# Optimization experiments

Measured on AMD Instinct MI355X. Metric: run time of the kernel, lower is better.

## Reference

```python
import jax, jax.numpy as jnp
import numpy as np

N, Q, C, T = 32, 300, 92, 32  # batch, queries, classes, targets-per-image
L_CLS, L_IOU, L_L1 = 1.0, 2.0, 5.0


def _cxcywh_to_xyxy(b):
    cx, cy, w, h = b[..., 0], b[..., 1], b[..., 2], b[..., 3]
    return jnp.stack([cx - 0.5 * w, cy - 0.5 * h, cx + 0.5 * w, cy + 0.5 * h], axis=-1)


def _generalized_box_iou(a, b):
    # a: [P,4] xyxy, b: [M,4] xyxy -> [P,M]
    area_a = (a[:, 2] - a[:, 0]) * (a[:, 3] - a[:, 1])
    area_b = (b[:, 2] - b[:, 0]) * (b[:, 3] - b[:, 1])
    lt = jnp.maximum(a[:, None, :2], b[None, :, :2])
    rb = jnp.minimum(a[:, None, 2:], b[None, :, 2:])
    wh = jnp.clip(rb - lt, 0.0)
    inter = wh[..., 0] * wh[..., 1]
    union = area_a[:, None] + area_b[None, :] - inter
    iou = inter / union
    lt_c = jnp.minimum(a[:, None, :2], b[None, :, :2])
    rb_c = jnp.maximum(a[:, None, 2:], b[None, :, 2:])
    wh_c = jnp.clip(rb_c - lt_c, 0.0)
    area_c = wh_c[..., 0] * wh_c[..., 1]
    return iou - (area_c - union) / area_c


def _cost_matrix(pred_logits, pred_boxes, tgt_labels, tgt_boxes):
    out_prob = jax.nn.softmax(pred_logits.reshape(-1, C), axis=-1)  # [N*Q, C]
    out_bbox = pred_boxes.reshape(-1, 4)                            # [N*Q, 4]
    cost_class = -out_prob[:, tgt_labels]                           # [N*Q, N*T]
    cost_bbox = jnp.sum(jnp.abs(out_bbox[:, None, :] - tgt_boxes[None, :, :]), axis=-1)
    cost_giou = -_generalized_box_iou(_cxcywh_to_xyxy(out_bbox), _cxcywh_to_xyxy(tgt_boxes))
    cost = L_L1 * cost_bbox + L_CLS * cost_class + L_IOU * cost_giou
    return cost.reshape(N, Q, N * T)


def _lsa(cost):
    # Jonker-Volgenant shortest augmenting path (e-maxx), cost: [n, m], n <= m.
    # Returns col4row: for each row, the assigned column.
    n, m = cost.shape
    INF = np.inf
    u = np.zeros(n + 1)
    v = np.zeros(m + 1)
    p = np.zeros(m + 1, dtype=np.int64)   # p[j] = row assigned to column j (1-based)
    way = np.zeros(m + 1, dtype=np.int64)
    for i in range(1, n + 1):
        p[0] = i
        j0 = 0
        minv = np.full(m + 1, INF)
        used = np.zeros(m + 1, dtype=bool)
        while True:
            used[j0] = True
            i0 = p[j0]
            free = ~used[1:]
            cur = cost[i0 - 1] - u[i0] - v[1:]
            upd = free & (cur < minv[1:])
            minv[1:][upd] = cur[upd]
            way[1:][upd] = j0
            j1 = 1 + int(np.argmin(np.where(free, minv[1:], INF)))
            delta = minv[j1]
            used_idx = np.nonzero(used)[0]
            u[p[used_idx]] += delta
            v[used_idx] -= delta
            minv[1:][free] -= delta
            j0 = j1
            if p[j0] == 0:
                break
        while j0:
            j1 = way[j0]
            p[j0] = p[j1]
            j0 = j1
    ans = np.full(n, -1, dtype=np.int64)
    js = np.nonzero(p[1:])[0]
    ans[p[1:][js] - 1] = js
    return ans


def _multiplier(cost):
    c_np = np.asarray(jax.device_get(cost))  # [N, Q, N*T]
    mult = np.zeros_like(c_np)
    for i in range(N):
        block = c_np[i, :, i * T:(i + 1) * T]  # [Q, T], sample i's own targets
        q_of_t = _lsa(block.T)                 # for each target, matched query
        # NOTE: faithfully replicates the original code's `count = 0` reset,
        # so columns are indexed locally (first T columns of the global axis).
        mult[i, q_of_t, np.arange(T)] = 1.0
    return jnp.asarray(mult)


def setup_inputs() -> dict:
    key = jax.random.key(0)
    k1, k2, k3, k4 = jax.random.split(key, 4)
    return {
        "pred_logits": jax.random.normal(k1, (N, Q, C), dtype=jnp.float32),
        "pred_boxes": jax.random.uniform(k2, (N, Q, 4), dtype=jnp.float32),
        "tgt_labels": jax.random.randint(k3, (N * T,), 0, C, dtype=jnp.int64),
        "tgt_boxes": jax.random.uniform(k4, (N * T, 4), dtype=jnp.float32),
    }


def reference(pred_logits, pred_boxes, tgt_labels, tgt_boxes):
    cost = _cost_matrix(pred_logits, pred_boxes, tgt_labels, tgt_boxes)
    mult = _multiplier(cost)
    return jnp.sum(cost * mult)
```

## Files before the change

kernel.cpp:

```cpp
#include <hip/hip_runtime.h>
#include <cfloat>
#include <cmath>

#define Nn 32
#define Qq 300
#define Cc 92
#define Tt 32
#define KCOLS 5
#define GSZ 10
#define GCOLS 30
#define AUCTION_ROUNDS 10
#define AUCTION_EPS 1e-3f

#define SLICES 8
#define RPS 38
#define CTHREADS 256
#define ATHREADS 320
#define FTHREADS 256

#define DIAG_OFF   0
#define MXIS_OFF   (Nn * Tt * Qq)
#define STATE_OFF  (MXIS_OFF + 2 * Nn * Qq)
#define STATE_STRIDE 640

__device__ inline float wave_min_bcast(float x) {
#define DPPMIN(ctrl) { int _t = __builtin_amdgcn_update_dpp( \
        __float_as_int(x), __float_as_int(x), ctrl, 0xf, 0xf, false); \
        x = fminf(x, __int_as_float(_t)); }
    DPPMIN(0x111) DPPMIN(0x112) DPPMIN(0x114) DPPMIN(0x118)
    DPPMIN(0x142) DPPMIN(0x143)
#undef DPPMIN
    return __int_as_float(__builtin_amdgcn_readlane(__float_as_int(x), 63));
}

__device__ inline int sel5i(const int a[KCOLS], int k) {
    int r = a[0];
    if (k == 1) r = a[1];
    if (k == 2) r = a[2];
    if (k == 3) r = a[3];
    if (k == 4) r = a[4];
    return r;
}

__device__ inline float readlane_f(float v, int lane) {
    return __int_as_float(__builtin_amdgcn_readlane(__float_as_int(v), lane));
}

__device__ inline float det_cost_real(float cx, float cy, float w, float h,
                                      float bcx, float bcy, float bw, float bh,
                                      float cls) {
    const float ax0 = cx - 0.5f * w, ay0 = cy - 0.5f * h;
    const float ax1 = cx + 0.5f * w, ay1 = cy + 0.5f * h;
    const float areaA = (ax1 - ax0) * (ay1 - ay0);

    const float l1 = fabsf(cx - bcx) + fabsf(cy - bcy) +
                     fabsf(w - bw) + fabsf(h - bh);

    const float bx0 = bcx - 0.5f * bw, by0 = bcy - 0.5f * bh;
    const float bx1 = bcx + 0.5f * bw, by1 = bcy + 0.5f * bh;
    const float areaB = (bx1 - bx0) * (by1 - by0);

    const float ltx = fmaxf(ax0, bx0), lty = fmaxf(ay0, by0);
    const float rbx = fminf(ax1, bx1), rby = fminf(ay1, by1);
    const float iw = fmaxf(rbx - ltx, 0.f), ih = fmaxf(rby - lty, 0.f);
    const float inter = iw * ih;
    const float uni = areaA + areaB - inter;
    const float iou = inter / uni;

    const float ex0 = fminf(ax0, bx0), ey0 = fminf(ay0, by0);
    const float ex1 = fmaxf(ax1, bx1), ey1 = fmaxf(ay1, by1);
    const float areaC = fmaxf(ex1 - ex0, 0.f) * fmaxf(ey1 - ey0, 0.f);
    const float giou = iou - (areaC - uni) / areaC;

    return 5.f * l1 + cls - 2.f * giou;
}

__global__ __launch_bounds__(CTHREADS) void cost_kernel(
    const float* __restrict__ logits,
    const float* __restrict__ pboxes,
    const int*   __restrict__ tlabels,
    const float* __restrict__ tboxes,
    float* __restrict__ ws)
{
    const int bs = blockIdx.x;
    const int b = bs >> 3, s = bs & 7;
    const int q0 = s * RPS;
    const int nq = min(RPS, Qq - q0);

    __shared__ float2 s_mxis[RPS];
    __shared__ float  s_tb[Tt * 4];
    __shared__ int    s_tl[Tt];

    const int tid = threadIdx.x;
    if (tid < Tt * 4) s_tb[tid] = tboxes[b * Tt * 4 + tid];
    if (tid < Tt)     s_tl[tid] = tlabels[b * Tt + tid];

    const int r = tid >> 2, j = tid & 3;
    if (r < nq) {
        const float* row = logits + ((size_t)(b * Qq) + q0 + r) * Cc;
        float mj = -FLT_MAX;
#pragma unroll
        for (int c = 0; c < Cc; c += 4) mj = fmaxf(mj, row[c + j]);
        const float ma = fmaxf(mj, __shfl_xor(mj, 1, 4));
        const float mx = fmaxf(ma, __shfl_xor(ma, 2, 4));
        float sj = 0.f;
#pragma unroll
        for (int c = 0; c < Cc; c += 4) sj += __expf(row[c + j] - mx);
        const float sa   = sj + __shfl_xor(sj, 1, 4);
        const float ssum = sa + __shfl_xor(sa, 2, 4);
        if (j == 0) {
            const float2 mi = make_float2(mx, 1.f / ssum);
            s_mxis[r] = mi;
            reinterpret_cast<float2*>(ws + MXIS_OFF)[b * Qq + q0 + r] = mi;
        }
    }
    __syncthreads();

    float* diagb = ws + DIAG_OFF + (size_t)b * (Tt * Qq);
    for (int e = tid; e < Tt * RPS; e += CTHREADS) {
        const int t = e / RPS, lq = e - t * RPS;
        const int q = q0 + lq;
        if (q < Qq) {
            const float2 mi = s_mxis[lq];
            const float cls =
                -__expf(logits[((size_t)(b * Qq) + q) * Cc + s_tl[t]] - mi.x) * mi.y;
            const float4 pbv = reinterpret_cast<const float4*>(pboxes)[b * Qq + q];
            diagb[t * Qq + q] = det_cost_real(pbv.x, pbv.y, pbv.z, pbv.w,
                                              s_tb[t * 4 + 0], s_tb[t * 4 + 1],
                                              s_tb[t * 4 + 2], s_tb[t * 4 + 3], cls);
        }
    }
}

__global__ __launch_bounds__(ATHREADS) void auction_kernel(
    float* __restrict__ ws)
{
    const int b = blockIdx.x;
    const int tid = threadIdx.x;

    __shared__ float s_diag[Tt * Qq];
    __shared__ float s_v[Qq];
    __shared__ float s_u[Tt + 1];
    __shared__ int   s_colrow[Qq];
    __shared__ unsigned long long s_bid64[Qq];
    __shared__ float s_pm1[ATHREADS], s_pm2[ATHREADS];
    __shared__ int   s_pa[ATHREADS];
    __shared__ unsigned s_mask;

    {
        const float4* src = reinterpret_cast<const float4*>(
            ws + DIAG_OFF + (size_t)b * (Tt * Qq));
        float4* dst = reinterpret_cast<float4*>(s_diag);
#pragma unroll 2
        for (int g = tid; g < (Tt * Qq) / 4; g += ATHREADS) dst[g] = src[g];
    }
    if (tid < Qq)  { s_v[tid] = 0.f; s_colrow[tid] = 0; }
    if (tid == 0)  s_mask = 0xffffffffu;
    __syncthreads();

    const int grp = tid / GSZ;
    const int g   = tid - grp * GSZ;
    for (int round = 0; round < AUCTION_ROUNDS; ++round) {
        const unsigned msk = s_mask;
        if (msk == 0) break;
        for (int jj = tid; jj < Qq; jj += ATHREADS) s_bid64[jj] = 0ull;

        if (grp < Tt && (msk & (1u << grp))) {
            const float* rowp = &s_diag[grp * Qq];
            float m1 = INFINITY, m2 = INFINITY; int a1 = 0;
            const int c0 = g * GCOLS;
#pragma unroll
            for (int jj = 0; jj < GCOLS; ++jj) {
                const int cidx = c0 + jj;
                const float c = rowp[cidx] - s_v[cidx];
                if (c < m1) { m2 = m1; m1 = c; a1 = cidx + 1; }
                else if (c < m2) m2 = c;
            }
            s_pm1[tid] = m1; s_pm2[tid] = m2; s_pa[tid] = a1;
        }
        __syncthreads();

        float g1 = 0.f, g2 = 0.f; int j1 = 0;
        unsigned long long mypk = 0ull;
        if (tid < Tt && (msk & (1u << tid))) {
            float best = INFINITY, second = INFINITY, bm2 = INFINITY;
            int ba = 0;
            const int base = tid * GSZ;
#pragma unroll
            for (int q = 0; q < GSZ; ++q) {
                const float v = s_pm1[base + q];
                if (v < best) {
                    second = best; best = v;
                    ba = s_pa[base + q]; bm2 = s_pm2[base + q];
                } else if (v < second) second = v;
            }
            g1 = best; g2 = fminf(second, bm2); j1 = ba;
            mypk = ((unsigned long long)(__float_as_uint(g2 - g1) + 1u) << 32)
                   | (unsigned)(0xffffffffu - (unsigned)(tid + 1));
            atomicMax(&s_bid64[j1 - 1], mypk);
        }
        __syncthreads();

        if (tid < Tt && (msk & (1u << tid))) {
            const int row = tid + 1;
            const float eps = (round < 2) ? 0.f : AUCTION_EPS;
            if (s_bid64[j1 - 1] == mypk) {
                const int old = s_colrow[j1 - 1];
                s_colrow[j1 - 1] = row;
                s_v[j1 - 1] -= (g2 - g1) + eps;
                s_u[row] = g2;
                atomicAnd(&s_mask, ~(1u << tid));
                if (old) atomicOr(&s_mask, 1u << (old - 1));
            } else {
                s_u[row] = g1;
            }
        }
        __syncthreads();
    }

    __syncthreads();
    float* st  = ws + STATE_OFF + (size_t)b * STATE_STRIDE;
    int*   sti = reinterpret_cast<int*>(st + 334);
    for (int jj = tid; jj < Qq; jj += ATHREADS) {
        st[jj]  = s_v[jj];
        sti[jj] = s_colrow[jj];
    }
    if (tid >= 1 && tid <= Tt) st[300 + tid] = s_u[tid];
    if (tid == 0) *reinterpret_cast<unsigned*>(st + 634) = s_mask;
}

__global__ __launch_bounds__(FTHREADS) void finish_kernel(
    const float* __restrict__ logits,
    const float* __restrict__ pboxes,
    const int*   __restrict__ tlabels,
    const float* __restrict__ tboxes,
    const float* __restrict__ ws,
    float* __restrict__ out)
{
    const int b = blockIdx.x;
    const int tid = threadIdx.x;

    __shared__ float s_diag[Tt * Qq];
    __shared__ int   pairs[Tt];

    {
        const float4* src = reinterpret_cast<const float4*>(
            ws + DIAG_OFF + (size_t)b * (Tt * Qq));
        float4* dst = reinterpret_cast<float4*>(s_diag);
#pragma unroll 2
        for (int g = tid; g < (Tt * Qq) / 4; g += FTHREADS) dst[g] = src[g];
    }
    __syncthreads();

    if (tid >= 64) return;
    const int lane = tid;
    const bool inval4 = (lane + 256) >= Qq;

    const float* st  = ws + STATE_OFF + (size_t)b * STATE_STRIDE;
    const int*   sti = reinterpret_cast<const int*>(st + 334);

    float u_reg = (lane >= 1 && lane <= Tt) ? st[300 + lane] : 0.f;
    float v_r[KCOLS]; int p_r[KCOLS];
#pragma unroll
    for (int k = 0; k < KCOLS; ++k) {
        const int jj = lane + 64 * k;
        v_r[k] = (jj < Qq) ? st[jj]  : 0.f;
        p_r[k] = (jj < Qq) ? sti[jj] : 0;
    }
    const unsigned mask0 = *reinterpret_cast<const unsigned*>(st + 634);

    for (unsigned rem = mask0; rem; rem &= rem - 1) {
        const int i = __ffs(rem);

        float minv_r[KCOLS], vmask[KCOLS], am[KCOLS];
        int way_r[KCOLS];
#pragma unroll
        for (int k = 0; k < KCOLS; ++k) {
            minv_r[k] = FLT_MAX; way_r[k] = 0;
            const bool inv = (k == 4) && inval4;
            vmask[k] = inv ? -INFINITY : v_r[k];
            am[k]    = inv ?  INFINITY : 0.f;
        }
        float markg = 0.f;
        int   ent = 0;
        int   j0 = 0, i0 = i;
        float du = 0.f - readlane_f(u_reg, i);
        int   jfinal = 0;
        float Dfinal = 0.f;

        const float* rowp = &s_diag[(i0 - 1) * Qq + lane];
        float c0 = rowp[0], c1 = rowp[64], c2 = rowp[128], c3 = rowp[192],
              c4 = rowp[256];

        while (true) {
            const float cc[KCOLS] = {c0, c1, c2, c3, c4};
            float sv[KCOLS];
#pragma unroll
            for (int k = 0; k < KCOLS; ++k) {
                const float cur = (cc[k] + du) - vmask[k];
                const bool lt = cur < minv_r[k];
                way_r[k]  = lt ? j0  : way_r[k];
                minv_r[k] = lt ? cur : minv_r[k];
                sv[k] = minv_r[k] + am[k];
            }
            float val = sv[0];
            int   kb  = 0;
#pragma unroll
            for (int k = 1; k < KCOLS; ++k)
                if (sv[k] < val) { val = sv[k]; kb = k; }

            const float gmin = wave_min_bcast(val);
            const unsigned long long mask = __ballot(val == gmin);
            const int src = __ffsll((long long)mask) - 1;
            const int colid = lane + 1 + (kb << 6);
            const int pk = (sel5i(p_r, kb) << 16) | colid;
            const int got = __builtin_amdgcn_readlane(pk, src);
            const int j1   = got & 0xffff;
            const int rowm = got >> 16;

            const int k1 = (j1 - 1) >> 6;
            const bool own = (lane == ((j1 - 1) & 63));
#pragma unroll
            for (int k = 0; k < KCOLS; ++k)
                if (own && k == k1) { vmask[k] = -INFINITY; am[k] = INFINITY; }

            if (rowm == 0) { jfinal = j1; Dfinal = gmin; break; }

            i0 = rowm; j0 = j1;
            rowp = &s_diag[(i0 - 1) * Qq + lane];
            c0 = rowp[0]; c1 = rowp[64]; c2 = rowp[128]; c3 = rowp[192];
            c4 = rowp[256];
            du = gmin - readlane_f(u_reg, i0);
            markg = (lane == rowm) ? gmin : markg;
            ent   = (lane == rowm) ? 1    : ent;
        }

#pragma unroll
        for (int k = 0; k < KCOLS; ++k) {
            bool usedk = (am[k] == INFINITY);
            if (k == 4) usedk = usedk && !inval4;
            v_r[k] -= usedk ? (Dfinal - minv_r[k]) : 0.f;
        }
        u_reg += (lane == i) ? Dfinal : (ent ? (Dfinal - markg) : 0.f);

        int jj = jfinal;
        while (jj) {
            const int ow = (jj - 1) & 63, kk = (jj - 1) >> 6;
            const int jprev = __builtin_amdgcn_readlane(sel5i(way_r, kk), ow);
            int pnew;
            if (jprev == 0) pnew = i;
            else pnew = __builtin_amdgcn_readlane(sel5i(p_r, (jprev - 1) >> 6),
                                                  (jprev - 1) & 63);
            const bool own = (lane == ow);
#pragma unroll
            for (int k = 0; k < KCOLS; ++k) if (own && k == kk) p_r[k] = pnew;
            jj = jprev;
        }
    }

#pragma unroll
    for (int k = 0; k < KCOLS; ++k)
        if (p_r[k]) pairs[p_r[k] - 1] = lane + 64 * k;
    __threadfence_block();

    float part = 0.f;
    if (lane < Tt) {
        const int q = pairs[lane];
        const float2 mi =
            reinterpret_cast<const float2*>(ws + MXIS_OFF)[b * Qq + q];
        const float cls =
            -__expf(logits[((size_t)(b * Qq) + q) * Cc + tlabels[lane]] - mi.x) * mi.y;
        const float4 pbv = reinterpret_cast<const float4*>(pboxes)[b * Qq + q];
        const float4 tbv = reinterpret_cast<const float4*>(tboxes)[lane];
        part = det_cost_real(pbv.x, pbv.y, pbv.z, pbv.w,
                             tbv.x, tbv.y, tbv.z, tbv.w, cls);
    }
    for (int off = 32; off > 0; off >>= 1) part += __shfl_down(part, off);
    if (lane == 0) atomicAdd(out, part);
}

extern "C" void kernel_launch(void* const* d_in, const int* in_sizes, int n_in,
                              void* d_out, int out_size, void* d_ws, size_t ws_size,
                              hipStream_t stream) {
    const float* logits  = (const float*)d_in[0];
    const float* pboxes  = (const float*)d_in[1];
    const int*   tlabels = (const int*)d_in[2];
    const float* tboxes  = (const float*)d_in[3];
    float* out = (float*)d_out;
    float* ws  = (float*)d_ws;

    (void)hipMemsetAsync(out, 0, sizeof(float), stream);
    cost_kernel<<<Nn * SLICES, CTHREADS, 0, stream>>>(logits, pboxes, tlabels,
                                                      tboxes, ws);
    auction_kernel<<<Nn, ATHREADS, 0, stream>>>(ws);
    finish_kernel<<<Nn, FTHREADS, 0, stream>>>(logits, pboxes, tlabels,
                                               tboxes, ws, out);
}
```

Baseline: 81.62 us.

## Fuse auction and finish kernels into one match kernel, drop memset

Merges the auction and Jonker-Volgenant finish kernels into a single per-image kernel. Dual prices, assignments and the unassigned mask now stay in shared memory instead of round-tripping through a global state buffer. This also removes one launch and the second global-to-LDS copy of the cost diagonal. The output is now zeroed inside cost_kernel instead of by a separate hipMemsetAsync, which relies on cost_kernel finishing before match_kernel adds to it.

```diff
diff --git a/kernel.cpp b/kernel.cpp
--- a/kernel.cpp
+++ b/kernel.cpp
@@ -15,13 +15,10 @@
 #define SLICES 8
 #define RPS 38
 #define CTHREADS 256
-#define ATHREADS 320
-#define FTHREADS 256
+#define MTHREADS 320
 
 #define DIAG_OFF   0
 #define MXIS_OFF   (Nn * Tt * Qq)
-#define STATE_OFF  (MXIS_OFF + 2 * Nn * Qq)
-#define STATE_STRIDE 640
 
 __device__ inline float wave_min_bcast(float x) {
 #define DPPMIN(ctrl) { int _t = __builtin_amdgcn_update_dpp( \
@@ -80,7 +77,8 @@
     const float* __restrict__ pboxes,
     const int*   __restrict__ tlabels,
     const float* __restrict__ tboxes,
-    float* __restrict__ ws)
+    float* __restrict__ ws,
+    float* __restrict__ out)
 {
     const int bs = blockIdx.x;
     const int b = bs >> 3, s = bs & 7;
@@ -92,6 +90,7 @@
     __shared__ int    s_tl[Tt];
 
     const int tid = threadIdx.x;
+    if (bs == 0 && tid == 0) *out = 0.f;
     if (tid < Tt * 4) s_tb[tid] = tboxes[b * Tt * 4 + tid];
     if (tid < Tt)     s_tl[tid] = tlabels[b * Tt + tid];
 
@@ -132,8 +131,13 @@
     }
 }
 
-__global__ __launch_bounds__(ATHREADS) void auction_kernel(
-    float* __restrict__ ws)
+__global__ __launch_bounds__(MTHREADS) void match_kernel(
+    const float* __restrict__ logits,
+    const float* __restrict__ pboxes,
+    const int*   __restrict__ tlabels,
+    const float* __restrict__ tboxes,
+    const float* __restrict__ ws,
+    float* __restrict__ out)
 {
     const int b = blockIdx.x;
     const int tid = threadIdx.x;
@@ -143,8 +147,9 @@
     __shared__ float s_u[Tt + 1];
     __shared__ int   s_colrow[Qq];
     __shared__ unsigned long long s_bid64[Qq];
-    __shared__ float s_pm1[ATHREADS], s_pm2[ATHREADS];
-    __shared__ int   s_pa[ATHREADS];
+    __shared__ float s_pm1[MTHREADS], s_pm2[MTHREADS];
+    __shared__ int   s_pa[MTHREADS];
+    __shared__ int   pairs[Tt];
     __shared__ unsigned s_mask;
 
     {
@@ -152,7 +157,7 @@
             ws + DIAG_OFF + (size_t)b * (Tt * Qq));
         float4* dst = reinterpret_cast<float4*>(s_diag);
 #pragma unroll 2
-        for (int g = tid; g < (Tt * Qq) / 4; g += ATHREADS) dst[g] = src[g];
+        for (int g = tid; g < (Tt * Qq) / 4; g += MTHREADS) dst[g] = src[g];
     }
     if (tid < Qq)  { s_v[tid] = 0.f; s_colrow[tid] = 0; }
     if (tid == 0)  s_mask = 0xffffffffu;
@@ -163,7 +168,7 @@
     for (int round = 0; round < AUCTION_ROUNDS; ++round) {
         const unsigned msk = s_mask;
         if (msk == 0) break;
-        for (int jj = tid; jj < Qq; jj += ATHREADS) s_bid64[jj] = 0ull;
+        for (int jj = tid; jj < Qq; jj += MTHREADS) s_bid64[jj] = 0ull;
 
         if (grp < Tt && (msk & (1u << grp))) {
             const float* rowp = &s_diag[grp * Qq];
@@ -218,56 +223,19 @@
         __syncthreads();
     }
 
-    __syncthreads();
-    float* st  = ws + STATE_OFF + (size_t)b * STATE_STRIDE;
-    int*   sti = reinterpret_cast<int*>(st + 334);
-    for (int jj = tid; jj < Qq; jj += ATHREADS) {
-        st[jj]  = s_v[jj];
-        sti[jj] = s_colrow[jj];
-    }
-    if (tid >= 1 && tid <= Tt) st[300 + tid] = s_u[tid];
-    if (tid == 0) *reinterpret_cast<unsigned*>(st + 634) = s_mask;
-}
-
-__global__ __launch_bounds__(FTHREADS) void finish_kernel(
-    const float* __restrict__ logits,
-    const float* __restrict__ pboxes,
-    const int*   __restrict__ tlabels,
-    const float* __restrict__ tboxes,
-    const float* __restrict__ ws,
-    float* __restrict__ out)
-{
-    const int b = blockIdx.x;
-    const int tid = threadIdx.x;
-
-    __shared__ float s_diag[Tt * Qq];
-    __shared__ int   pairs[Tt];
-
-    {
-        const float4* src = reinterpret_cast<const float4*>(
-            ws + DIAG_OFF + (size_t)b * (Tt * Qq));
-        float4* dst = reinterpret_cast<float4*>(s_diag);
-#pragma unroll 2
-        for (int g = tid; g < (Tt * Qq) / 4; g += FTHREADS) dst[g] = src[g];
-    }
-    __syncthreads();
-
     if (tid >= 64) return;
     const int lane = tid;
     const bool inval4 = (lane + 256) >= Qq;
 
-    const float* st  = ws + STATE_OFF + (size_t)b * STATE_STRIDE;
-    const int*   sti = reinterpret_cast<const int*>(st + 334);
-
-    float u_reg = (lane >= 1 && lane <= Tt) ? st[300 + lane] : 0.f;
+    float u_reg = (lane >= 1 && lane <= Tt) ? s_u[lane] : 0.f;
     float v_r[KCOLS]; int p_r[KCOLS];
 #pragma unroll
     for (int k = 0; k < KCOLS; ++k) {
         const int jj = lane + 64 * k;
-        v_r[k] = (jj < Qq) ? st[jj]  : 0.f;
-        p_r[k] = (jj < Qq) ? sti[jj] : 0;
-    }
-    const unsigned mask0 = *reinterpret_cast<const unsigned*>(st + 634);
+        v_r[k] = (jj < Qq) ? s_v[jj] : 0.f;
+        p_r[k] = (jj < Qq) ? s_colrow[jj] : 0;
+    }
+    const unsigned mask0 = s_mask;
 
     for (unsigned rem = mask0; rem; rem &= rem - 1) {
         const int i = __ffs(rem);
@@ -389,10 +357,8 @@
     float* out = (float*)d_out;
     float* ws  = (float*)d_ws;
 
-    (void)hipMemsetAsync(out, 0, sizeof(float), stream);
     cost_kernel<<<Nn * SLICES, CTHREADS, 0, stream>>>(logits, pboxes, tlabels,
-                                                      tboxes, ws);
-    auction_kernel<<<Nn, ATHREADS, 0, stream>>>(ws);
-    finish_kernel<<<Nn, FTHREADS, 0, stream>>>(logits, pboxes, tlabels,
-                                               tboxes, ws, out);
-}
+                                                      tboxes, ws, out);
+    match_kernel<<<Nn, MTHREADS, 0, stream>>>(logits, pboxes, tlabels,
+                                              tboxes, ws, out);
+}
```

Result: faster. 77.73 us (-4.8%).
